# Kernel optimization log

Hardware: AMD Instinct MI355X
Metric: run time of the kernel (lower is better)

## Reference

```python
import jax, jax.numpy as jnp
import numpy as np

B, H, S, D = 2, 16, 2048, 128

def setup_inputs() -> dict:
    key = jax.random.key(0)
    k1, k2, k3 = jax.random.split(key, 3)
    return {
        "input": jax.random.normal(k1, (B, H, S, D), dtype=jnp.float32),
        "weight": jax.random.normal(k2, (B, H, S, D), dtype=jnp.float32),
        "value": jax.random.normal(k3, (B, H, S, D), dtype=jnp.float32),
    }

def reference(input, weight, value):
    # qk = input @ weight^T  -> [B, H, S, S]
    qk = jnp.einsum("bhqd,bhkd->bhqk", input, weight)
    scaled_qk = qk / 1.0  # div(1) no-op kept for fidelity
    softmax_qk = jax.nn.softmax(scaled_qk, axis=-1)
    # dropout is identity in eval mode (deterministic baseline)
    out = jnp.einsum("bhqk,bhkd->bhqd", softmax_qk, value)
    return out
```

## Files before the change

kernel.cpp:

```cpp
#include <hip/hip_runtime.h>
#include <hip/hip_bf16.h>

typedef __attribute__((ext_vector_type(8)))  _Float16 half8;
typedef __attribute__((ext_vector_type(2)))  _Float16 half2v;
typedef __attribute__((ext_vector_type(16))) float f32x16;
typedef __attribute__((ext_vector_type(4)))  unsigned int uint4v;
typedef __attribute__((ext_vector_type(2)))  unsigned int uint2v;
typedef unsigned int   uint32;
typedef unsigned short u16;

#define DEV __device__ __forceinline__

constexpr int S   = 2048;
constexpr int D   = 128;
constexpr int BH  = 32;
constexpr int QB  = 128;
constexpr int KVB = 64;
constexpr int NT  = S / KVB;
constexpr float LOG2E = 1.4426950408889634f;
constexpr size_t WS_NEED = (size_t)2 * BH * S * D * sizeof(u16);

DEV uint32 pk2(float a, float b) {
  half2v h = { (_Float16)a, (_Float16)b };
  return __builtin_bit_cast(uint32, h);
}
DEV u16 tof16(float a) {
  _Float16 h = (_Float16)a;
  return __builtin_bit_cast(u16, h);
}
DEV float f4c(const float4& v, int c) {
  return c == 0 ? v.x : c == 1 ? v.y : c == 2 ? v.z : v.w;
}
DEV float partner32(float x, int h) {
  uint2v r = __builtin_amdgcn_permlane32_swap(
      __builtin_bit_cast(uint32, x), __builtin_bit_cast(uint32, x), false, false);
  return __builtin_bit_cast(float, h ? r[0] : r[1]);
}
DEV void gl2lds16(const void* g, void* l) {
  __builtin_amdgcn_global_load_lds(
      (const __attribute__((address_space(1))) void*)g,
      (__attribute__((address_space(3))) void*)l, 16, 0, 0);
}

__global__ __launch_bounds__(256)
void k_to_half(const float* __restrict__ Kg, u16* __restrict__ Kh) {
  const int n4 = BH * S * D / 4;
  for (int i = blockIdx.x * 256 + threadIdx.x; i < n4; i += gridDim.x * 256) {
    float4 v = ((const float4*)Kg)[i];
    uint2v p = { pk2(v.x, v.y), pk2(v.z, v.w) };
    *(uint2v*)(Kh + (size_t)i * 4) = p;
  }
}

__global__ __launch_bounds__(256)
void v_transpose(const float* __restrict__ Vg, u16* __restrict__ Vt) {
  __shared__ u16 tile[64][72];
  const int tid = threadIdx.x;
  int b = blockIdx.x;
  const int dt = b & 1;  b >>= 1;
  const int st = b & 31; b >>= 5;
  const int bh = b;
  const int s0 = st * 64, d0 = dt * 64;
  const float* Vb = Vg + (size_t)bh * S * D;
  const int j = tid & 63;
  #pragma unroll
  for (int ii = 0; ii < 16; ++ii) {
    const int i = (tid >> 6) * 16 + ii;
    tile[i][j] = tof16(Vb[(size_t)(s0 + i) * D + d0 + j]);
  }
  __syncthreads();
  u16* Vtb = Vt + (size_t)bh * D * S;
  const int jd = tid >> 2;
  const int q  = tid & 3;
  #pragma unroll
  for (int s4 = 0; s4 < 4; ++s4) {
    const int si = q * 16 + s4 * 4;
    uint2v pv = { (uint32)tile[si + 0][jd] | ((uint32)tile[si + 1][jd] << 16),
                  (uint32)tile[si + 2][jd] | ((uint32)tile[si + 3][jd] << 16) };
    *(uint2v*)(Vtb + (size_t)(d0 + jd) * S + s0 + si) = pv;
  }
}

__global__ __launch_bounds__(256, 2)
void attn_fwd(const float* __restrict__ Qg, const u16* __restrict__ Kh,
              const u16* __restrict__ Vt, float* __restrict__ Og) {
  __shared__ __align__(16) char kb[2][64 * 256];
  __shared__ __align__(16) char vb[2][64 * 256];

  const int tid = threadIdx.x;
  const int w  = tid >> 6;
  const int l  = tid & 63;
  const int lo = l & 31;
  const int h  = l >> 5;

  const int idb = blockIdx.x;
  const int swz = (idb & 7) * 64 + (idb >> 3);
  const int bh  = swz >> 4;
  const int qb  = swz & 15;

  const size_t base = (size_t)bh * S * D;
  const float4* __restrict__ Q4 = (const float4*)(Qg + base);
  const u16* __restrict__ Ks = Kh + base;
  const u16* __restrict__ Vs = Vt + base;

  half8 qf[8];
  {
    const int q = qb * QB + w * 32 + lo;
    #pragma unroll
    for (int kc = 0; kc < 8; ++kc) {
      const int f4 = q * 32 + kc * 4 + h * 2;
      float4 a = Q4[f4];
      float4 b = Q4[f4 + 1];
      uint4v uu = { pk2(a.x, a.y), pk2(a.z, a.w), pk2(b.x, b.y), pk2(b.z, b.w) };
      qf[kc] = __builtin_bit_cast(half8, uu);
    }
  }

  f32x16 acc0 = {}, acc1 = {}, acc2 = {}, acc3 = {};
  float m_run = -3.0e38f, l_run = 0.f;

  const int srow0 = tid >> 4;
  const int sg    = tid & 15;

  auto stage = [&](int t, int bsel) {
    const u16* kt = Ks + (size_t)t * KVB * D;
    const u16* vt = Vs + (size_t)t * KVB;
    char* kd = kb[bsel] + w * 1024;
    char* vd = vb[bsel] + w * 1024;
    #pragma unroll
    for (int i = 0; i < 4; ++i) {
      const int r  = i * 16 + srow0;
      const int gu = sg ^ (r & 15);
      gl2lds16(kt + r * D + gu * 8, kd + i * 4096);
    }
    #pragma unroll
    for (int i = 0; i < 4; ++i) {
      const int r  = i * 16 + srow0;
      const int gu = sg ^ (r & 15);
      const int d  = r + ((gu >> 3) << 6);
      gl2lds16(vt + (size_t)d * S + ((gu & 7) << 3), vd + i * 4096);
    }
  };

  stage(0, 0);
  stage(1, 1);
  asm volatile("s_waitcnt vmcnt(0)" ::: "memory");
  __syncthreads();

  for (int t = 0; t < NT; ++t) {
    const int cur = t & 1;
    const char* kcur = kb[cur];
    const char* vcur = vb[cur];

    f32x16 st0 = {}, st1 = {};
    __builtin_amdgcn_s_setprio(1);
    #pragma unroll
    for (int kc = 0; kc < 8; ++kc) {
      const int boff = kc * 32 + h * 16;
      const int sw = (lo & 15) << 4;
      half8 kf0 = *(const half8*)(kcur + lo * 256        + (boff ^ sw));
      half8 kf1 = *(const half8*)(kcur + (32 + lo) * 256 + (boff ^ sw));
      st0 = __builtin_amdgcn_mfma_f32_32x32x16_f16(kf0, qf[kc], st0, 0, 0, 0);
      st1 = __builtin_amdgcn_mfma_f32_32x32x16_f16(kf1, qf[kc], st1, 0, 0, 0);
    }
    __builtin_amdgcn_s_setprio(0);

    float mA = fmaxf(st0[0], st1[0]), mB = fmaxf(st0[1], st1[1]);
    float mC = fmaxf(st0[2], st1[2]), mD = fmaxf(st0[3], st1[3]);
    #pragma unroll
    for (int r = 4; r < 16; r += 4) {
      mA = fmaxf(mA, fmaxf(st0[r],   st1[r]));
      mB = fmaxf(mB, fmaxf(st0[r+1], st1[r+1]));
      mC = fmaxf(mC, fmaxf(st0[r+2], st1[r+2]));
      mD = fmaxf(mD, fmaxf(st0[r+3], st1[r+3]));
    }
    float mloc = fmaxf(fmaxf(mA, mB), fmaxf(mC, mD));
    mloc = fmaxf(mloc, partner32(mloc, h));

    if (!__all(mloc - m_run <= 8.0f)) {
      const float m_new = fmaxf(m_run, mloc);
      const float alpha = exp2f((m_run - m_new) * LOG2E);
      l_run *= alpha;
      #pragma unroll
      for (int r = 0; r < 16; ++r) {
        acc0[r] *= alpha; acc1[r] *= alpha; acc2[r] *= alpha; acc3[r] *= alpha;
      }
      m_run = m_new;
    }
    const float mm = m_run * LOG2E;

    float sA = 0.f, sB = 0.f, sC = 0.f, sD = 0.f;
    #pragma unroll
    for (int r = 0; r < 16; r += 4) {
      st0[r]   = exp2f(st0[r]   * LOG2E - mm); sA += st0[r];
      st0[r+1] = exp2f(st0[r+1] * LOG2E - mm); sB += st0[r+1];
      st0[r+2] = exp2f(st0[r+2] * LOG2E - mm); sC += st0[r+2];
      st0[r+3] = exp2f(st0[r+3] * LOG2E - mm); sD += st0[r+3];
      st1[r]   = exp2f(st1[r]   * LOG2E - mm); sA += st1[r];
      st1[r+1] = exp2f(st1[r+1] * LOG2E - mm); sB += st1[r+1];
      st1[r+2] = exp2f(st1[r+2] * LOG2E - mm); sC += st1[r+2];
      st1[r+3] = exp2f(st1[r+3] * LOG2E - mm); sD += st1[r+3];
    }
    float lsum = (sA + sB) + (sC + sD);
    lsum += partner32(lsum, h);
    l_run += lsum;

    half8 pb[4];
    #define PACK_KS(SRC, RB, DST) { \
      uint32 u01 = pk2(SRC[RB+0], SRC[RB+1]); \
      uint32 u23 = pk2(SRC[RB+2], SRC[RB+3]); \
      uint32 v01 = pk2(SRC[RB+4], SRC[RB+5]); \
      uint32 v23 = pk2(SRC[RB+6], SRC[RB+7]); \
      uint2v r01 = __builtin_amdgcn_permlane32_swap(u01, v01, false, false); \
      uint2v r23 = __builtin_amdgcn_permlane32_swap(u23, v23, false, false); \
      uint4v uu = { r01[0], r23[0], r01[1], r23[1] }; \
      DST = __builtin_bit_cast(half8, uu); }
    PACK_KS(st0, 0, pb[0])
    PACK_KS(st0, 8, pb[1])
    PACK_KS(st1, 0, pb[2])
    PACK_KS(st1, 8, pb[3])
    #undef PACK_KS

    __builtin_amdgcn_s_setprio(1);
    #pragma unroll
    for (int ks = 0; ks < 4; ++ks) {
      #define PVSTEP(DT, ACC) { \
        const int rr  = DT * 32 + lo; \
        const int row = rr & 63; \
        const int gu  = ((rr >> 6) << 3) + ks * 2 + h; \
        half8 vf = *(const half8*)(vcur + row * 256 + ((gu ^ (row & 15)) << 4)); \
        ACC = __builtin_amdgcn_mfma_f32_32x32x16_f16(vf, pb[ks], ACC, 0, 0, 0); }
      PVSTEP(0, acc0) PVSTEP(1, acc1) PVSTEP(2, acc2) PVSTEP(3, acc3)
      #undef PVSTEP
    }
    __builtin_amdgcn_s_setprio(0);

    asm volatile("s_waitcnt vmcnt(0)" ::: "memory");
    __syncthreads();
    if (t + 2 < NT) stage(t + 2, cur);
  }

  const float rl = 1.0f / l_run;
  const int q = qb * QB + w * 32 + lo;
  float* Op = Og + base + (size_t)q * D;
  auto store_dt = [&](int dt, const f32x16& a) {
    #pragma unroll
    for (int rq = 0; rq < 4; ++rq) {
      float4 o = { a[rq*4+0]*rl, a[rq*4+1]*rl, a[rq*4+2]*rl, a[rq*4+3]*rl };
      *(float4*)(Op + dt * 32 + rq * 8 + h * 4) = o;
    }
  };
  store_dt(0, acc0); store_dt(1, acc1); store_dt(2, acc2); store_dt(3, acc3);
}

__global__ __launch_bounds__(256, 2)
void attn_fwd_fb(const float* __restrict__ Qg, const float* __restrict__ Kg,
                 const float* __restrict__ Vg, float* __restrict__ Og) {
  __shared__ __align__(16) char kb[2][64 * 256];
  __shared__ __align__(16) char vb[2][128 * 128];
  const int tid = threadIdx.x;
  const int w = tid >> 6, l = tid & 63, lo = l & 31, h = l >> 5;
  const int idb = blockIdx.x;
  const int swz = (idb & 7) * 64 + (idb >> 3);
  const int bh = swz >> 4, qb = swz & 15;
  const size_t base = (size_t)bh * S * D;
  const float4* __restrict__ Q4 = (const float4*)(Qg + base);
  const float4* __restrict__ K4 = (const float4*)(Kg + base);
  const float4* __restrict__ V4 = (const float4*)(Vg + base);
  half8 qf[8];
  {
    const int q = qb * QB + w * 32 + lo;
    #pragma unroll
    for (int kc = 0; kc < 8; ++kc) {
      const int f4 = q * 32 + kc * 4 + h * 2;
      float4 a = Q4[f4]; float4 b = Q4[f4 + 1];
      uint4v uu = { pk2(a.x, a.y), pk2(a.z, a.w), pk2(b.x, b.y), pk2(b.z, b.w) };
      qf[kc] = __builtin_bit_cast(half8, uu);
    }
  }
  f32x16 acc0 = {}, acc1 = {}, acc2 = {}, acc3 = {};
  float m_run = -3.0e38f, l_run = 0.f;
  const int kr = tid & 63, kq = tid >> 6;
  const int vkv4 = (tid & 15) * 4, vdb = tid >> 4;
  float4 kreg[8], vreg[8];
  auto stage_issue = [&](int t) {
    const int r0 = t * KVB;
    #pragma unroll
    for (int i = 0; i < 8; ++i) kreg[i] = K4[(r0 + kr) * 32 + kq * 8 + i];
    #pragma unroll
    for (int k = 0; k < 4; ++k)
      #pragma unroll
      for (int i = 0; i < 2; ++i)
        vreg[k * 2 + i] = V4[(r0 + vkv4 + k) * 32 + vdb * 2 + i];
  };
  auto stage_write = [&](int bsel) {
    char* kd = kb[bsel]; char* vd = vb[bsel];
    #pragma unroll
    for (int i2 = 0; i2 < 4; ++i2) {
      const float4 a = kreg[2 * i2], b = kreg[2 * i2 + 1];
      uint4v uu = { pk2(a.x, a.y), pk2(a.z, a.w), pk2(b.x, b.y), pk2(b.z, b.w) };
      *(uint4v*)(kd + kr * 256 + ((kq * 64 + i2 * 16) ^ ((kr & 7) << 4))) = uu;
    }
    #pragma unroll
    for (int p = 0; p < 8; ++p) {
      const int i = p >> 2, c = p & 3;
      const int d = vdb * 8 + p;
      uint2v pv = { pk2(f4c(vreg[0 + i], c), f4c(vreg[2 + i], c)),
                    pk2(f4c(vreg[4 + i], c), f4c(vreg[6 + i], c)) };
      *(uint2v*)(vd + d * 128 + ((vkv4 * 2) ^ ((d & 7) << 4))) = pv;
    }
  };
  stage_issue(0); stage_write(0); __syncthreads();
  for (int t = 0; t < NT; ++t) {
    const char* kcur = kb[t & 1]; const char* vcur = vb[t & 1];
    f32x16 st0 = {}, st1 = {};
    #pragma unroll
    for (int kc = 0; kc < 8; ++kc) {
      const int boff = kc * 32 + h * 16;
      const int sw = (lo & 7) << 4;
      half8 kf0 = *(const half8*)(kcur + lo * 256        + (boff ^ sw));
      half8 kf1 = *(const half8*)(kcur + (32 + lo) * 256 + (boff ^ sw));
      st0 = __builtin_amdgcn_mfma_f32_32x32x16_f16(kf0, qf[kc], st0, 0, 0, 0);
      st1 = __builtin_amdgcn_mfma_f32_32x32x16_f16(kf1, qf[kc], st1, 0, 0, 0);
    }
    if (t + 1 < NT) stage_issue(t + 1);
    float mA = fmaxf(st0[0], st1[0]), mB = fmaxf(st0[1], st1[1]);
    float mC = fmaxf(st0[2], st1[2]), mD = fmaxf(st0[3], st1[3]);
    #pragma unroll
    for (int r = 4; r < 16; r += 4) {
      mA = fmaxf(mA, fmaxf(st0[r],   st1[r]));
      mB = fmaxf(mB, fmaxf(st0[r+1], st1[r+1]));
      mC = fmaxf(mC, fmaxf(st0[r+2], st1[r+2]));
      mD = fmaxf(mD, fmaxf(st0[r+3], st1[r+3]));
    }
    float mloc = fmaxf(fmaxf(mA, mB), fmaxf(mC, mD));
    mloc = fmaxf(mloc, partner32(mloc, h));
    if (!__all(mloc - m_run <= 8.0f)) {
      const float m_new = fmaxf(m_run, mloc);
      const float alpha = exp2f((m_run - m_new) * LOG2E);
      l_run *= alpha;
      #pragma unroll
      for (int r = 0; r < 16; ++r) {
        acc0[r] *= alpha; acc1[r] *= alpha; acc2[r] *= alpha; acc3[r] *= alpha;
      }
      m_run = m_new;
    }
    const float mm = m_run * LOG2E;
    float sA = 0.f, sB = 0.f, sC = 0.f, sD = 0.f;
    #pragma unroll
    for (int r = 0; r < 16; r += 4) {
      st0[r]   = exp2f(st0[r]   * LOG2E - mm); sA += st0[r];
      st0[r+1] = exp2f(st0[r+1] * LOG2E - mm); sB += st0[r+1];
      st0[r+2] = exp2f(st0[r+2] * LOG2E - mm); sC += st0[r+2];
      st0[r+3] = exp2f(st0[r+3] * LOG2E - mm); sD += st0[r+3];
      st1[r]   = exp2f(st1[r]   * LOG2E - mm); sA += st1[r];
      st1[r+1] = exp2f(st1[r+1] * LOG2E - mm); sB += st1[r+1];
      st1[r+2] = exp2f(st1[r+2] * LOG2E - mm); sC += st1[r+2];
      st1[r+3] = exp2f(st1[r+3] * LOG2E - mm); sD += st1[r+3];
    }
    float lsum = (sA + sB) + (sC + sD);
    lsum += partner32(lsum, h);
    l_run += lsum;
    half8 pb[4];
    #define PACK_KS(SRC, RB, DST) { \
      uint32 u01 = pk2(SRC[RB+0], SRC[RB+1]); \
      uint32 u23 = pk2(SRC[RB+2], SRC[RB+3]); \
      uint32 v01 = pk2(SRC[RB+4], SRC[RB+5]); \
      uint32 v23 = pk2(SRC[RB+6], SRC[RB+7]); \
      uint2v r01 = __builtin_amdgcn_permlane32_swap(u01, v01, false, false); \
      uint2v r23 = __builtin_amdgcn_permlane32_swap(u23, v23, false, false); \
      uint4v uu = { r01[0], r23[0], r01[1], r23[1] }; \
      DST = __builtin_bit_cast(half8, uu); }
    PACK_KS(st0, 0, pb[0]) PACK_KS(st0, 8, pb[1])
    PACK_KS(st1, 0, pb[2]) PACK_KS(st1, 8, pb[3])
    #undef PACK_KS
    #pragma unroll
    for (int ks = 0; ks < 4; ++ks) {
      const int boff = ks * 32 + h * 16;
      #define PVSTEP(DT, ACC) { const int rr = DT * 32 + lo; \
        half8 vf = *(const half8*)(vcur + rr * 128 + (boff ^ ((rr & 7) << 4))); \
        ACC = __builtin_amdgcn_mfma_f32_32x32x16_f16(vf, pb[ks], ACC, 0, 0, 0); }
      PVSTEP(0, acc0) PVSTEP(1, acc1) PVSTEP(2, acc2) PVSTEP(3, acc3)
      #undef PVSTEP
    }
    if (t + 1 < NT) stage_write((t + 1) & 1);
    __syncthreads();
  }
  const float rl = 1.0f / l_run;
  const int q = qb * QB + w * 32 + lo;
  float* Op = Og + base + (size_t)q * D;
  auto store_dt = [&](int dt, const f32x16& a) {
    #pragma unroll
    for (int rq = 0; rq < 4; ++rq) {
      float4 o = { a[rq*4+0]*rl, a[rq*4+1]*rl, a[rq*4+2]*rl, a[rq*4+3]*rl };
      *(float4*)(Op + dt * 32 + rq * 8 + h * 4) = o;
    }
  };
  store_dt(0, acc0); store_dt(1, acc1); store_dt(2, acc2); store_dt(3, acc3);
}

extern "C" void kernel_launch(void* const* d_in, const int* in_sizes, int n_in,
                              void* d_out, int out_size, void* d_ws, size_t ws_size,
                              hipStream_t stream) {
  (void)in_sizes; (void)n_in; (void)out_size;
  const float* Q = (const float*)d_in[0];
  const float* K = (const float*)d_in[1];
  const float* V = (const float*)d_in[2];
  float* O = (float*)d_out;
  if (ws_size >= WS_NEED) {
    u16* Kh = (u16*)d_ws;
    u16* Vt = Kh + (size_t)BH * S * D;
    k_to_half<<<dim3(1024), dim3(256), 0, stream>>>(K, Kh);
    v_transpose<<<dim3(2048), dim3(256), 0, stream>>>(V, Vt);
    attn_fwd<<<dim3(512), dim3(256), 0, stream>>>(Q, Kh, Vt, O);
  } else {
    attn_fwd_fb<<<dim3(512), dim3(256), 0, stream>>>(Q, K, V, O);
  }
}
```

Baseline: 118.1 us.

## Software-pipeline QK of next tile with softmax/PV of current tile

```diff
diff --git a/kernel.cpp b/kernel.cpp
--- a/kernel.cpp
+++ b/kernel.cpp
@@ -111,7 +111,8 @@
       const int f4 = q * 32 + kc * 4 + h * 2;
       float4 a = Q4[f4];
       float4 b = Q4[f4 + 1];
-      uint4v uu = { pk2(a.x, a.y), pk2(a.z, a.w), pk2(b.x, b.y), pk2(b.z, b.w) };
+      uint4v uu = { pk2(a.x * LOG2E, a.y * LOG2E), pk2(a.z * LOG2E, a.w * LOG2E),
+                    pk2(b.x * LOG2E, b.y * LOG2E), pk2(b.z * LOG2E, b.w * LOG2E) };
       qf[kc] = __builtin_bit_cast(half8, uu);
     }
   }
@@ -122,17 +123,19 @@
   const int srow0 = tid >> 4;
   const int sg    = tid & 15;
 
-  auto stage = [&](int t, int bsel) {
+  auto stageK = [&](int t, int bsel) {
     const u16* kt = Ks + (size_t)t * KVB * D;
-    const u16* vt = Vs + (size_t)t * KVB;
     char* kd = kb[bsel] + w * 1024;
-    char* vd = vb[bsel] + w * 1024;
     #pragma unroll
     for (int i = 0; i < 4; ++i) {
       const int r  = i * 16 + srow0;
       const int gu = sg ^ (r & 15);
       gl2lds16(kt + r * D + gu * 8, kd + i * 4096);
     }
+  };
+  auto stageV = [&](int t, int bsel) {
+    const u16* vt = Vs + (size_t)t * KVB;
+    char* vd = vb[bsel] + w * 1024;
     #pragma unroll
     for (int i = 0; i < 4; ++i) {
       const int r  = i * 16 + srow0;
@@ -142,17 +145,9 @@
     }
   };
 
-  stage(0, 0);
-  stage(1, 1);
-  asm volatile("s_waitcnt vmcnt(0)" ::: "memory");
-  __syncthreads();
-
-  for (int t = 0; t < NT; ++t) {
-    const int cur = t & 1;
-    const char* kcur = kb[cur];
-    const char* vcur = vb[cur];
-
-    f32x16 st0 = {}, st1 = {};
+  auto qk = [&](int bsel, f32x16& SN0, f32x16& SN1) {
+    const char* kcur = kb[bsel];
+    SN0 = {}; SN1 = {};
     __builtin_amdgcn_s_setprio(1);
     #pragma unroll
     for (int kc = 0; kc < 8; ++kc) {
@@ -160,85 +155,108 @@
       const int sw = (lo & 15) << 4;
       half8 kf0 = *(const half8*)(kcur + lo * 256        + (boff ^ sw));
       half8 kf1 = *(const half8*)(kcur + (32 + lo) * 256 + (boff ^ sw));
-      st0 = __builtin_amdgcn_mfma_f32_32x32x16_f16(kf0, qf[kc], st0, 0, 0, 0);
-      st1 = __builtin_amdgcn_mfma_f32_32x32x16_f16(kf1, qf[kc], st1, 0, 0, 0);
+      SN0 = __builtin_amdgcn_mfma_f32_32x32x16_f16(kf0, qf[kc], SN0, 0, 0, 0);
+      SN1 = __builtin_amdgcn_mfma_f32_32x32x16_f16(kf1, qf[kc], SN1, 0, 0, 0);
     }
     __builtin_amdgcn_s_setprio(0);
-
-    float mA = fmaxf(st0[0], st1[0]), mB = fmaxf(st0[1], st1[1]);
-    float mC = fmaxf(st0[2], st1[2]), mD = fmaxf(st0[3], st1[3]);
-    #pragma unroll
-    for (int r = 4; r < 16; r += 4) {
-      mA = fmaxf(mA, fmaxf(st0[r],   st1[r]));
-      mB = fmaxf(mB, fmaxf(st0[r+1], st1[r+1]));
-      mC = fmaxf(mC, fmaxf(st0[r+2], st1[r+2]));
-      mD = fmaxf(mD, fmaxf(st0[r+3], st1[r+3]));
-    }
-    float mloc = fmaxf(fmaxf(mA, mB), fmaxf(mC, mD));
-    mloc = fmaxf(mloc, partner32(mloc, h));
-
-    if (!__all(mloc - m_run <= 8.0f)) {
-      const float m_new = fmaxf(m_run, mloc);
-      const float alpha = exp2f((m_run - m_new) * LOG2E);
-      l_run *= alpha;
-      #pragma unroll
-      for (int r = 0; r < 16; ++r) {
-        acc0[r] *= alpha; acc1[r] *= alpha; acc2[r] *= alpha; acc3[r] *= alpha;
-      }
-      m_run = m_new;
-    }
-    const float mm = m_run * LOG2E;
-
-    float sA = 0.f, sB = 0.f, sC = 0.f, sD = 0.f;
-    #pragma unroll
-    for (int r = 0; r < 16; r += 4) {
-      st0[r]   = exp2f(st0[r]   * LOG2E - mm); sA += st0[r];
-      st0[r+1] = exp2f(st0[r+1] * LOG2E - mm); sB += st0[r+1];
-      st0[r+2] = exp2f(st0[r+2] * LOG2E - mm); sC += st0[r+2];
-      st0[r+3] = exp2f(st0[r+3] * LOG2E - mm); sD += st0[r+3];
-      st1[r]   = exp2f(st1[r]   * LOG2E - mm); sA += st1[r];
-      st1[r+1] = exp2f(st1[r+1] * LOG2E - mm); sB += st1[r+1];
-      st1[r+2] = exp2f(st1[r+2] * LOG2E - mm); sC += st1[r+2];
-      st1[r+3] = exp2f(st1[r+3] * LOG2E - mm); sD += st1[r+3];
-    }
-    float lsum = (sA + sB) + (sC + sD);
-    lsum += partner32(lsum, h);
-    l_run += lsum;
-
-    half8 pb[4];
-    #define PACK_KS(SRC, RB, DST) { \
-      uint32 u01 = pk2(SRC[RB+0], SRC[RB+1]); \
-      uint32 u23 = pk2(SRC[RB+2], SRC[RB+3]); \
-      uint32 v01 = pk2(SRC[RB+4], SRC[RB+5]); \
-      uint32 v23 = pk2(SRC[RB+6], SRC[RB+7]); \
-      uint2v r01 = __builtin_amdgcn_permlane32_swap(u01, v01, false, false); \
-      uint2v r23 = __builtin_amdgcn_permlane32_swap(u23, v23, false, false); \
-      uint4v uu = { r01[0], r23[0], r01[1], r23[1] }; \
-      DST = __builtin_bit_cast(half8, uu); }
-    PACK_KS(st0, 0, pb[0])
-    PACK_KS(st0, 8, pb[1])
-    PACK_KS(st1, 0, pb[2])
-    PACK_KS(st1, 8, pb[3])
-    #undef PACK_KS
-
-    __builtin_amdgcn_s_setprio(1);
-    #pragma unroll
-    for (int ks = 0; ks < 4; ++ks) {
-      #define PVSTEP(DT, ACC) { \
-        const int rr  = DT * 32 + lo; \
-        const int row = rr & 63; \
-        const int gu  = ((rr >> 6) << 3) + ks * 2 + h; \
-        half8 vf = *(const half8*)(vcur + row * 256 + ((gu ^ (row & 15)) << 4)); \
-        ACC = __builtin_amdgcn_mfma_f32_32x32x16_f16(vf, pb[ks], ACC, 0, 0, 0); }
-      PVSTEP(0, acc0) PVSTEP(1, acc1) PVSTEP(2, acc2) PVSTEP(3, acc3)
-      #undef PVSTEP
-    }
-    __builtin_amdgcn_s_setprio(0);
-
-    asm volatile("s_waitcnt vmcnt(0)" ::: "memory");
-    __syncthreads();
-    if (t + 2 < NT) stage(t + 2, cur);
-  }
+  };
+
+  stageK(0, 0); stageV(0, 0);
+  stageK(1, 1); stageV(1, 1);
+  asm volatile("s_waitcnt vmcnt(0)" ::: "memory");
+  __syncthreads();
+  f32x16 stA0, stA1, stB0, stB1;
+  qk(0, stA0, stA1);
+  __syncthreads();
+
+  #define BODY(T, SC0, SC1, SN0, SN1)                                          \
+  {                                                                            \
+    const int cur = (T) & 1, nxt = cur ^ 1;                                    \
+    if ((T) + 2 < NT) stageK((T) + 2, cur);                                    \
+    if ((T) + 1 < NT) qk(nxt, SN0, SN1);                                       \
+                                    \
+    float mA = fmaxf(SC0[0], SC1[0]), mB = fmaxf(SC0[1], SC1[1]);              \
+    float mC = fmaxf(SC0[2], SC1[2]), mD = fmaxf(SC0[3], SC1[3]);              \
+    _Pragma("unroll")                                                          \
+    for (int r = 4; r < 16; r += 4) {                                          \
+      mA = fmaxf(mA, fmaxf(SC0[r],   SC1[r]));                                 \
+      mB = fmaxf(mB, fmaxf(SC0[r+1], SC1[r+1]));                               \
+      mC = fmaxf(mC, fmaxf(SC0[r+2], SC1[r+2]));                               \
+      mD = fmaxf(mD, fmaxf(SC0[r+3], SC1[r+3]));                               \
+    }                                                                          \
+    float mloc = fmaxf(fmaxf(mA, mB), fmaxf(mC, mD));                          \
+    mloc = fmaxf(mloc, partner32(mloc, h));                                    \
+    if (!__all(mloc - m_run <= 8.0f)) {                                        \
+      const float m_new = fmaxf(m_run, mloc);                                  \
+      const float alpha = exp2f(m_run - m_new);                                \
+      l_run *= alpha;                                                          \
+      _Pragma("unroll")                                                        \
+      for (int r = 0; r < 16; ++r) {                                           \
+        acc0[r] *= alpha; acc1[r] *= alpha; acc2[r] *= alpha; acc3[r] *= alpha;\
+      }                                                                        \
+      m_run = m_new;                                                           \
+    }                                                                          \
+    const float mm = m_run;                                                    \
+    float sA = 0.f, sB = 0.f, sC = 0.f, sD = 0.f;                              \
+    _Pragma("unroll")                                                          \
+    for (int r = 0; r < 16; r += 4) {                                          \
+      SC0[r]   = exp2f(SC0[r]   - mm); sA += SC0[r];                           \
+      SC0[r+1] = exp2f(SC0[r+1] - mm); sB += SC0[r+1];                         \
+      SC0[r+2] = exp2f(SC0[r+2] - mm); sC += SC0[r+2];                         \
+      SC0[r+3] = exp2f(SC0[r+3] - mm); sD += SC0[r+3];                         \
+      SC1[r]   = exp2f(SC1[r]   - mm); sA += SC1[r];                           \
+      SC1[r+1] = exp2f(SC1[r+1] - mm); sB += SC1[r+1];                         \
+      SC1[r+2] = exp2f(SC1[r+2] - mm); sC += SC1[r+2];                         \
+      SC1[r+3] = exp2f(SC1[r+3] - mm); sD += SC1[r+3];                         \
+    }                                                                          \
+    float lsum = (sA + sB) + (sC + sD);                                        \
+    lsum += partner32(lsum, h);                                                \
+    l_run += lsum;                                                             \
+                                             \
+    half8 pb[4];                                                               \
+    PACK_KS(SC0, 0, pb[0])                                                     \
+    PACK_KS(SC0, 8, pb[1])                                                     \
+    PACK_KS(SC1, 0, pb[2])                                                     \
+    PACK_KS(SC1, 8, pb[3])                                                     \
+                                               \
+    {                                                                          \
+      const char* vcur = vb[cur];                                              \
+      __builtin_amdgcn_s_setprio(1);                                           \
+      _Pragma("unroll")                                                        \
+      for (int ks = 0; ks < 4; ++ks) {                                         \
+        PVSTEP(0, acc0) PVSTEP(1, acc1) PVSTEP(2, acc2) PVSTEP(3, acc3)        \
+      }                                                                        \
+      __builtin_amdgcn_s_setprio(0);                                           \
+    }                                                                          \
+    asm volatile("s_waitcnt vmcnt(0)" ::: "memory");                           \
+    __syncthreads();                                                           \
+    if ((T) + 2 < NT) stageV((T) + 2, cur);                                    \
+  }
+
+  #define PACK_KS(SRC, RB, DST) {                                              \
+    uint32 u01 = pk2(SRC[RB+0], SRC[RB+1]);                                    \
+    uint32 u23 = pk2(SRC[RB+2], SRC[RB+3]);                                    \
+    uint32 v01 = pk2(SRC[RB+4], SRC[RB+5]);                                    \
+    uint32 v23 = pk2(SRC[RB+6], SRC[RB+7]);                                    \
+    uint2v r01 = __builtin_amdgcn_permlane32_swap(u01, v01, false, false);     \
+    uint2v r23 = __builtin_amdgcn_permlane32_swap(u23, v23, false, false);     \
+    uint4v uu = { r01[0], r23[0], r01[1], r23[1] };                            \
+    DST = __builtin_bit_cast(half8, uu); }
+
+  #define PVSTEP(DT, ACC) {                                                    \
+    const int rr  = DT * 32 + lo;                                              \
+    const int row = rr & 63;                                                   \
+    const int gu  = ((rr >> 6) << 3) + ks * 2 + h;                             \
+    half8 vf = *(const half8*)(vcur + row * 256 + ((gu ^ (row & 15)) << 4));   \
+    ACC = __builtin_amdgcn_mfma_f32_32x32x16_f16(vf, pb[ks], ACC, 0, 0, 0); }
+
+  for (int t = 0; t < NT; t += 2) {
+    BODY(t,     stA0, stA1, stB0, stB1)
+    BODY(t + 1, stB0, stB1, stA0, stA1)
+  }
+  #undef BODY
+  #undef PACK_KS
+  #undef PVSTEP
 
   const float rl = 1.0f / l_run;
   const int q = qb * QB + w * 32 + lo;
```

New measurement: 117.9 us. No clear change (-0.2%).

## Split KV sequence across two wave groups per block and merge partial softmax

Applied to the files above, without the earlier changes.

```diff
diff --git a/kernel.cpp b/kernel.cpp
--- a/kernel.cpp
+++ b/kernel.cpp
@@ -15,8 +15,8 @@
 constexpr int D   = 128;
 constexpr int BH  = 32;
 constexpr int QB  = 128;
-constexpr int KVB = 64;
-constexpr int NT  = S / KVB;
+constexpr int KVG = 32;
+constexpr int NTG = (S / 2) / KVG;
 constexpr float LOG2E = 1.4426950408889634f;
 constexpr size_t WS_NEED = (size_t)2 * BH * S * D * sizeof(u16);
 
@@ -81,17 +81,22 @@
   }
 }
 
-__global__ __launch_bounds__(256, 2)
+__global__ __launch_bounds__(512, 4)
 void attn_fwd(const float* __restrict__ Qg, const u16* __restrict__ Kh,
               const u16* __restrict__ Vt, float* __restrict__ Og) {
-  __shared__ __align__(16) char kb[2][64 * 256];
-  __shared__ __align__(16) char vb[2][64 * 256];
-
-  const int tid = threadIdx.x;
-  const int w  = tid >> 6;
-  const int l  = tid & 63;
-  const int lo = l & 31;
-  const int h  = l >> 5;
+  __shared__ __align__(16) char kb[2][2][32 * 256];
+  __shared__ __align__(16) char vb[2][2][32 * 256];
+
+  const int tid  = threadIdx.x;
+  const int w    = tid >> 6;
+  const int l    = tid & 63;
+  const int lo   = l & 31;
+  const int h    = l >> 5;
+  const int g    = w >> 2;
+  const int wq   = w & 3;
+  const int ltid = tid & 255;
+  const int sg   = ltid & 15;
+  const int kvbase = g << 10;
 
   const int idb = blockIdx.x;
   const int swz = (idb & 7) * 64 + (idb >> 3);
@@ -105,13 +110,14 @@
 
   half8 qf[8];
   {
-    const int q = qb * QB + w * 32 + lo;
+    const int q = qb * QB + wq * 32 + lo;
     #pragma unroll
     for (int kc = 0; kc < 8; ++kc) {
       const int f4 = q * 32 + kc * 4 + h * 2;
       float4 a = Q4[f4];
       float4 b = Q4[f4 + 1];
-      uint4v uu = { pk2(a.x, a.y), pk2(a.z, a.w), pk2(b.x, b.y), pk2(b.z, b.w) };
+      uint4v uu = { pk2(a.x * LOG2E, a.y * LOG2E), pk2(a.z * LOG2E, a.w * LOG2E),
+                    pk2(b.x * LOG2E, b.y * LOG2E), pk2(b.z * LOG2E, b.w * LOG2E) };
       qf[kc] = __builtin_bit_cast(half8, uu);
     }
   }
@@ -119,26 +125,22 @@
   f32x16 acc0 = {}, acc1 = {}, acc2 = {}, acc3 = {};
   float m_run = -3.0e38f, l_run = 0.f;
 
-  const int srow0 = tid >> 4;
-  const int sg    = tid & 15;
-
   auto stage = [&](int t, int bsel) {
-    const u16* kt = Ks + (size_t)t * KVB * D;
-    const u16* vt = Vs + (size_t)t * KVB;
-    char* kd = kb[bsel] + w * 1024;
-    char* vd = vb[bsel] + w * 1024;
-    #pragma unroll
-    for (int i = 0; i < 4; ++i) {
-      const int r  = i * 16 + srow0;
+    const int kv0 = kvbase + t * KVG;
+    char* kd = kb[g][bsel] + wq * 1024;
+    char* vd = vb[g][bsel] + wq * 1024;
+    #pragma unroll
+    for (int i = 0; i < 2; ++i) {
+      const int r  = i * 16 + (ltid >> 4);
       const int gu = sg ^ (r & 15);
-      gl2lds16(kt + r * D + gu * 8, kd + i * 4096);
-    }
-    #pragma unroll
-    for (int i = 0; i < 4; ++i) {
-      const int r  = i * 16 + srow0;
+      gl2lds16(Ks + (size_t)(kv0 + r) * D + gu * 8, kd + i * 4096);
+    }
+    #pragma unroll
+    for (int i = 0; i < 2; ++i) {
+      const int r  = i * 16 + (ltid >> 4);
       const int gu = sg ^ (r & 15);
-      const int d  = r + ((gu >> 3) << 6);
-      gl2lds16(vt + (size_t)d * S + ((gu & 7) << 3), vd + i * 4096);
+      const int d  = r + ((gu >> 2) << 5);
+      gl2lds16(Vs + (size_t)d * S + kv0 + ((gu & 3) << 3), vd + i * 4096);
     }
   };
 
@@ -147,39 +149,33 @@
   asm volatile("s_waitcnt vmcnt(0)" ::: "memory");
   __syncthreads();
 
-  for (int t = 0; t < NT; ++t) {
+  for (int t = 0; t < NTG; ++t) {
     const int cur = t & 1;
-    const char* kcur = kb[cur];
-    const char* vcur = vb[cur];
-
-    f32x16 st0 = {}, st1 = {};
+    const char* kcur = kb[g][cur];
+    const char* vcur = vb[g][cur];
+
+    f32x16 st = {};
     __builtin_amdgcn_s_setprio(1);
     #pragma unroll
     for (int kc = 0; kc < 8; ++kc) {
       const int boff = kc * 32 + h * 16;
-      const int sw = (lo & 15) << 4;
-      half8 kf0 = *(const half8*)(kcur + lo * 256        + (boff ^ sw));
-      half8 kf1 = *(const half8*)(kcur + (32 + lo) * 256 + (boff ^ sw));
-      st0 = __builtin_amdgcn_mfma_f32_32x32x16_f16(kf0, qf[kc], st0, 0, 0, 0);
-      st1 = __builtin_amdgcn_mfma_f32_32x32x16_f16(kf1, qf[kc], st1, 0, 0, 0);
+      half8 kf = *(const half8*)(kcur + lo * 256 + (boff ^ ((lo & 15) << 4)));
+      st = __builtin_amdgcn_mfma_f32_32x32x16_f16(kf, qf[kc], st, 0, 0, 0);
     }
     __builtin_amdgcn_s_setprio(0);
 
-    float mA = fmaxf(st0[0], st1[0]), mB = fmaxf(st0[1], st1[1]);
-    float mC = fmaxf(st0[2], st1[2]), mD = fmaxf(st0[3], st1[3]);
+    float mA = st[0], mB = st[1], mC = st[2], mD = st[3];
     #pragma unroll
     for (int r = 4; r < 16; r += 4) {
-      mA = fmaxf(mA, fmaxf(st0[r],   st1[r]));
-      mB = fmaxf(mB, fmaxf(st0[r+1], st1[r+1]));
-      mC = fmaxf(mC, fmaxf(st0[r+2], st1[r+2]));
-      mD = fmaxf(mD, fmaxf(st0[r+3], st1[r+3]));
+      mA = fmaxf(mA, st[r]);   mB = fmaxf(mB, st[r+1]);
+      mC = fmaxf(mC, st[r+2]); mD = fmaxf(mD, st[r+3]);
     }
     float mloc = fmaxf(fmaxf(mA, mB), fmaxf(mC, mD));
     mloc = fmaxf(mloc, partner32(mloc, h));
 
     if (!__all(mloc - m_run <= 8.0f)) {
       const float m_new = fmaxf(m_run, mloc);
-      const float alpha = exp2f((m_run - m_new) * LOG2E);
+      const float alpha = exp2f(m_run - m_new);
       l_run *= alpha;
       #pragma unroll
       for (int r = 0; r < 16; ++r) {
@@ -187,47 +183,43 @@
       }
       m_run = m_new;
     }
-    const float mm = m_run * LOG2E;
+    const float mm = m_run;
 
     float sA = 0.f, sB = 0.f, sC = 0.f, sD = 0.f;
     #pragma unroll
     for (int r = 0; r < 16; r += 4) {
-      st0[r]   = exp2f(st0[r]   * LOG2E - mm); sA += st0[r];
-      st0[r+1] = exp2f(st0[r+1] * LOG2E - mm); sB += st0[r+1];
-      st0[r+2] = exp2f(st0[r+2] * LOG2E - mm); sC += st0[r+2];
-      st0[r+3] = exp2f(st0[r+3] * LOG2E - mm); sD += st0[r+3];
-      st1[r]   = exp2f(st1[r]   * LOG2E - mm); sA += st1[r];
-      st1[r+1] = exp2f(st1[r+1] * LOG2E - mm); sB += st1[r+1];
-      st1[r+2] = exp2f(st1[r+2] * LOG2E - mm); sC += st1[r+2];
-      st1[r+3] = exp2f(st1[r+3] * LOG2E - mm); sD += st1[r+3];
+      st[r]   = exp2f(st[r]   - mm); sA += st[r];
+      st[r+1] = exp2f(st[r+1] - mm); sB += st[r+1];
+      st[r+2] = exp2f(st[r+2] - mm); sC += st[r+2];
+      st[r+3] = exp2f(st[r+3] - mm); sD += st[r+3];
     }
     float lsum = (sA + sB) + (sC + sD);
     lsum += partner32(lsum, h);
     l_run += lsum;
 
-    half8 pb[4];
-    #define PACK_KS(SRC, RB, DST) { \
-      uint32 u01 = pk2(SRC[RB+0], SRC[RB+1]); \
-      uint32 u23 = pk2(SRC[RB+2], SRC[RB+3]); \
-      uint32 v01 = pk2(SRC[RB+4], SRC[RB+5]); \
-      uint32 v23 = pk2(SRC[RB+6], SRC[RB+7]); \
-      uint2v r01 = __builtin_amdgcn_permlane32_swap(u01, v01, false, false); \
-      uint2v r23 = __builtin_amdgcn_permlane32_swap(u23, v23, false, false); \
-      uint4v uu = { r01[0], r23[0], r01[1], r23[1] }; \
-      DST = __builtin_bit_cast(half8, uu); }
-    PACK_KS(st0, 0, pb[0])
-    PACK_KS(st0, 8, pb[1])
-    PACK_KS(st1, 0, pb[2])
-    PACK_KS(st1, 8, pb[3])
-    #undef PACK_KS
+    half8 pb[2];
+    {
+      uint32 u01 = pk2(st[0], st[1]),  u23 = pk2(st[2], st[3]);
+      uint32 v01 = pk2(st[4], st[5]),  v23 = pk2(st[6], st[7]);
+      uint2v r01 = __builtin_amdgcn_permlane32_swap(u01, v01, false, false);
+      uint2v r23 = __builtin_amdgcn_permlane32_swap(u23, v23, false, false);
+      uint4v uu = { r01[0], r23[0], r01[1], r23[1] };
+      pb[0] = __builtin_bit_cast(half8, uu);
+      uint32 x01 = pk2(st[8], st[9]),  x23 = pk2(st[10], st[11]);
+      uint32 y01 = pk2(st[12], st[13]), y23 = pk2(st[14], st[15]);
+      uint2v s01 = __builtin_amdgcn_permlane32_swap(x01, y01, false, false);
+      uint2v s23 = __builtin_amdgcn_permlane32_swap(x23, y23, false, false);
+      uint4v vv = { s01[0], s23[0], s01[1], s23[1] };
+      pb[1] = __builtin_bit_cast(half8, vv);
+    }
 
     __builtin_amdgcn_s_setprio(1);
     #pragma unroll
-    for (int ks = 0; ks < 4; ++ks) {
+    for (int ks = 0; ks < 2; ++ks) {
       #define PVSTEP(DT, ACC) { \
         const int rr  = DT * 32 + lo; \
-        const int row = rr & 63; \
-        const int gu  = ((rr >> 6) << 3) + ks * 2 + h; \
+        const int row = rr & 31; \
+        const int gu  = ((rr >> 5) << 2) + ks * 2 + h; \
         half8 vf = *(const half8*)(vcur + row * 256 + ((gu ^ (row & 15)) << 4)); \
         ACC = __builtin_amdgcn_mfma_f32_32x32x16_f16(vf, pb[ks], ACC, 0, 0, 0); }
       PVSTEP(0, acc0) PVSTEP(1, acc1) PVSTEP(2, acc2) PVSTEP(3, acc3)
@@ -237,20 +229,60 @@
 
     asm volatile("s_waitcnt vmcnt(0)" ::: "memory");
     __syncthreads();
-    if (t + 2 < NT) stage(t + 2, cur);
-  }
-
-  const float rl = 1.0f / l_run;
-  const int q = qb * QB + w * 32 + lo;
-  float* Op = Og + base + (size_t)q * D;
-  auto store_dt = [&](int dt, const f32x16& a) {
-    #pragma unroll
-    for (int rq = 0; rq < 4; ++rq) {
-      float4 o = { a[rq*4+0]*rl, a[rq*4+1]*rl, a[rq*4+2]*rl, a[rq*4+3]*rl };
-      *(float4*)(Op + dt * 32 + rq * 8 + h * 4) = o;
-    }
-  };
-  store_dt(0, acc0); store_dt(1, acc1); store_dt(2, acc2); store_dt(3, acc3);
+    if (t + 2 < NTG) stage(t + 2, cur);
+  }
+
+  float* mlb = (float*)vb;
+  float* ab  = (float*)kb;
+  if (g == 1) {
+    mlb[ltid * 2]     = m_run;
+    mlb[ltid * 2 + 1] = l_run;
+    #pragma unroll
+    for (int r = 0; r < 16; ++r) {
+      ab[r * 256 + ltid]        = acc0[r];
+      ab[(16 + r) * 256 + ltid] = acc1[r];
+    }
+  }
+  __syncthreads();
+  float a0 = 0.f, a1 = 0.f, rl = 0.f;
+  if (g == 0) {
+    const float m1 = mlb[ltid * 2], l1 = mlb[ltid * 2 + 1];
+    const float m  = fmaxf(m_run, m1);
+    a0 = exp2f(m_run - m);
+    a1 = exp2f(m1 - m);
+    rl = 1.0f / (l_run * a0 + l1 * a1);
+    #pragma unroll
+    for (int r = 0; r < 16; ++r) {
+      acc0[r] = acc0[r] * a0 + ab[r * 256 + ltid] * a1;
+      acc1[r] = acc1[r] * a0 + ab[(16 + r) * 256 + ltid] * a1;
+    }
+  }
+  __syncthreads();
+  if (g == 1) {
+    #pragma unroll
+    for (int r = 0; r < 16; ++r) {
+      ab[r * 256 + ltid]        = acc2[r];
+      ab[(16 + r) * 256 + ltid] = acc3[r];
+    }
+  }
+  __syncthreads();
+  if (g == 0) {
+    #pragma unroll
+    for (int r = 0; r < 16; ++r) {
+      acc2[r] = acc2[r] * a0 + ab[r * 256 + ltid] * a1;
+      acc3[r] = acc3[r] * a0 + ab[(16 + r) * 256 + ltid] * a1;
+    }
+    const int q = qb * QB + wq * 32 + lo;
+    float* Op = Og + base + (size_t)q * D;
+    auto store_dt = [&](int dt, const f32x16& a) {
+      #pragma unroll
+      for (int rq = 0; rq < 4; ++rq) {
+        float4 o = { a[rq*4+0]*rl, a[rq*4+1]*rl, a[rq*4+2]*rl, a[rq*4+3]*rl };
+        *(float4*)(Op + dt * 32 + rq * 8 + h * 4) = o;
+      }
+    };
+    store_dt(0, acc0); store_dt(1, acc1); store_dt(2, acc2); store_dt(3, acc3);
+  }
 }
 
 __global__ __launch_bounds__(256, 2)
@@ -269,7 +301,7 @@
   const float4* __restrict__ V4 = (const float4*)(Vg + base);
   half8 qf[8];
   {
-    const int q = qb * QB + w * 32 + lo;
+    const int q = qb * 128 + w * 32 + lo;
     #pragma unroll
     for (int kc = 0; kc < 8; ++kc) {
       const int f4 = q * 32 + kc * 4 + h * 2;
@@ -284,7 +316,7 @@
   const int vkv4 = (tid & 15) * 4, vdb = tid >> 4;
   float4 kreg[8], vreg[8];
   auto stage_issue = [&](int t) {
-    const int r0 = t * KVB;
+    const int r0 = t * 64;
     #pragma unroll
     for (int i = 0; i < 8; ++i) kreg[i] = K4[(r0 + kr) * 32 + kq * 8 + i];
     #pragma unroll
@@ -311,7 +343,7 @@
     }
   };
   stage_issue(0); stage_write(0); __syncthreads();
-  for (int t = 0; t < NT; ++t) {
+  for (int t = 0; t < 32; ++t) {
     const char* kcur = kb[t & 1]; const char* vcur = vb[t & 1];
     f32x16 st0 = {}, st1 = {};
     #pragma unroll
@@ -323,7 +355,7 @@
       st0 = __builtin_amdgcn_mfma_f32_32x32x16_f16(kf0, qf[kc], st0, 0, 0, 0);
       st1 = __builtin_amdgcn_mfma_f32_32x32x16_f16(kf1, qf[kc], st1, 0, 0, 0);
     }
-    if (t + 1 < NT) stage_issue(t + 1);
+    if (t + 1 < 32) stage_issue(t + 1);
     float mA = fmaxf(st0[0], st1[0]), mB = fmaxf(st0[1], st1[1]);
     float mC = fmaxf(st0[2], st1[2]), mD = fmaxf(st0[3], st1[3]);
     #pragma unroll
@@ -383,11 +415,11 @@
       PVSTEP(0, acc0) PVSTEP(1, acc1) PVSTEP(2, acc2) PVSTEP(3, acc3)
       #undef PVSTEP
     }
-    if (t + 1 < NT) stage_write((t + 1) & 1);
+    if (t + 1 < 32) stage_write((t + 1) & 1);
     __syncthreads();
   }
   const float rl = 1.0f / l_run;
-  const int q = qb * QB + w * 32 + lo;
+  const int q = qb * 128 + w * 32 + lo;
   float* Op = Og + base + (size_t)q * D;
   auto store_dt = [&](int dt, const f32x16& a) {
     #pragma unroll
@@ -412,7 +444,7 @@
     u16* Vt = Kh + (size_t)BH * S * D;
     k_to_half<<<dim3(1024), dim3(256), 0, stream>>>(K, Kh);
     v_transpose<<<dim3(2048), dim3(256), 0, stream>>>(V, Vt);
-    attn_fwd<<<dim3(512), dim3(256), 0, stream>>>(Q, Kh, Vt, O);
+    attn_fwd<<<dim3(512), dim3(512), 0, stream>>>(Q, Kh, Vt, O);
   } else {
     attn_fwd_fb<<<dim3(512), dim3(256), 0, stream>>>(Q, K, V, O);
   }
```

Result: slower. 155.7 us (+31.8%).
